# Kernel tuning notes

Measured on AMD Instinct MI355X. Metric: run time of the kernel, lower is better.

The kernel has to match this reference:

```python
import jax, jax.numpy as jnp
import numpy as np

D_MODEL = 1024
NUM_HEADS = 16
D_K = D_MODEL // NUM_HEADS


def setup_inputs() -> dict:
    key = jax.random.key(0)
    ks = jax.random.split(key, 11)
    B, S = 2, 2048
    scale = 1.0 / np.sqrt(D_MODEL)
    inp = {
        "q": jax.random.normal(ks[0], (B, S, D_MODEL), jnp.float32),
        "k": jax.random.normal(ks[1], (B, S, D_MODEL), jnp.float32),
        "v": jax.random.normal(ks[2], (B, S, D_MODEL), jnp.float32),
        "wq": jax.random.normal(ks[3], (D_MODEL, D_MODEL), jnp.float32) * scale,
        "bq": jax.random.normal(ks[4], (D_MODEL,), jnp.float32) * 0.01,
        "wk": jax.random.normal(ks[5], (D_MODEL, D_MODEL), jnp.float32) * scale,
        "bk": jax.random.normal(ks[6], (D_MODEL,), jnp.float32) * 0.01,
        "wv": jax.random.normal(ks[7], (D_MODEL, D_MODEL), jnp.float32) * scale,
        "bv": jax.random.normal(ks[8], (D_MODEL,), jnp.float32) * 0.01,
        "wo": jax.random.normal(ks[9], (D_MODEL, D_MODEL), jnp.float32) * scale,
        "bo": jax.random.normal(ks[10], (D_MODEL,), jnp.float32) * 0.01,
    }
    return inp


def reference(q, k, v, wq, bq, wk, bk, wv, bv, wo, bo):
    B, S, _ = q.shape
    # Linear projections (torch Linear: x @ W.T + b). Weights stored [out, in].
    qh = (q @ wq.T + bq).reshape(B, S, NUM_HEADS, D_K).transpose(0, 2, 1, 3)  # [B,H,S,dk]
    kh = (k @ wk.T + bk).reshape(B, S, NUM_HEADS, D_K).transpose(0, 2, 1, 3)
    vh = (v @ wv.T + bv).reshape(B, S, NUM_HEADS, D_K).transpose(0, 2, 1, 3)
    scores = jnp.einsum("bhqd,bhkd->bhqk", qh, kh) / jnp.sqrt(jnp.asarray(D_K, qh.dtype))
    weights = jax.nn.softmax(scores, axis=-1)
    attn = jnp.einsum("bhqk,bhkd->bhqd", weights, vh)  # [B,H,S,dk]
    attn = attn.transpose(0, 2, 1, 3).reshape(B, S, D_MODEL)
    return attn @ wo.T + bo
```

## Files before the change

kernel.cpp:

```cpp
#include <hip/hip_runtime.h>

#define DM 1024
#define NH 16
#define DK 64
#define BB 2
#define SS 2048
#define MT (BB*SS)

typedef __attribute__((ext_vector_type(8))) short bf16x8;
typedef __attribute__((ext_vector_type(4))) float f32x4;

#define QSCALE 0.1803368801111191f
#define EXPC  (-14.426950408889634f)

__device__ __forceinline__ unsigned short f2bf(float f) {
    unsigned int u = __float_as_uint(f);
    u += 0x7FFF + ((u >> 16) & 1);
    return (unsigned short)(u >> 16);
}

__device__ __forceinline__ unsigned int cvt_pk_bf16(float lo, float hi) {
    unsigned int r;
    asm("v_cvt_pk_bf16_f32 %0, %1, %2" : "=v"(r) : "v"(lo), "v"(hi));
    return r;
}

__device__ __forceinline__ void gload16(const void* g, void* l) {
    __builtin_amdgcn_global_load_lds(
        (const __attribute__((address_space(1))) unsigned int*)g,
        (__attribute__((address_space(3))) unsigned int*)(unsigned int)(unsigned long long)l,
        16, 0, 0);
}

__device__ __forceinline__ int kperm(int s) {
    return (s & ~31) | (((s >> 2) & 1) << 4) | (((s >> 3) & 3) << 2) | (s & 3);
}

struct CvtArgs {
    const float* s[7];
    unsigned short* d[7];
    int n[7];
    float scl[7];
};

__global__ __launch_bounds__(256) void cvt_f32_bf16(CvtArgs a) {
    const int arr = blockIdx.y;
    const int i = (blockIdx.x * 256 + threadIdx.x) * 8;
    if (i >= a.n[arr]) return;
    const float sc = a.scl[arr];
    const float4* sp = (const float4*)(a.s[arr] + i);
    float4 x = sp[0], y = sp[1];
    union { unsigned short us[8]; uint4 u4; } r;
    r.us[0] = f2bf(x.x * sc); r.us[1] = f2bf(x.y * sc);
    r.us[2] = f2bf(x.z * sc); r.us[3] = f2bf(x.w * sc);
    r.us[4] = f2bf(y.x * sc); r.us[5] = f2bf(y.y * sc);
    r.us[6] = f2bf(y.z * sc); r.us[7] = f2bf(y.w * sc);
    *(uint4*)(a.d[arr] + i) = r.u4;
}

struct ProjArgs {
    const unsigned short* A[3];
    const unsigned short* B[3];
    const float* bias[3];
    unsigned short* out[3];
    float bscale[3];
};

__global__ __launch_bounds__(256, 3) void proj3(ProjArgs pa) {
    __shared__ __align__(16) unsigned short As[2][128 * 32];
    __shared__ __align__(16) unsigned short Bs[2][128 * 32];

    const int z = blockIdx.y;
    const int bx = blockIdx.x;
    const int m0 = (z < 2 ? (bx >> 3) : (bx >> 5)) * 128;
    const int n0 = (z < 2 ? (bx & 7) : (bx & 31)) * 128;
    const unsigned short* A = pa.A[z];
    const unsigned short* B = pa.B[z];
    const float* bias = pa.bias[z];
    const float bsc = pa.bscale[z];
    unsigned short* out = pa.out[z];

    const int tid = (int)threadIdx.x;
    const int l = tid & 63;
    const int w = tid >> 6;
    const int wm = w >> 1, wn = w & 1;

    const int strow = l >> 2;
    const int sslot = (l & 3) ^ ((l >> 3) & 3);
    const int fr = l & 15, fj = l >> 4;
    const int swz = ((fj ^ ((fr >> 1) & 3)) << 4);

    const f32x4 zero = {0.f, 0.f, 0.f, 0.f};
    f32x4 acc[4][4];
    #pragma unroll
    for (int mf = 0; mf < 4; ++mf)
        #pragma unroll
        for (int nf = 0; nf < 4; ++nf) acc[mf][nf] = zero;

    #pragma unroll
    for (int t = 0; t < 2; ++t) {
        const int c = w * 2 + t;
        const int row = c * 16 + strow;
        gload16(A + (size_t)(m0 + row) * DM + sslot * 8, (char*)As[0] + c * 1024);
        gload16(B + (size_t)(n0 + row) * DM + sslot * 8, (char*)Bs[0] + c * 1024);
    }
    __syncthreads();

    for (int kt = 0; kt < DM; kt += 32) {
        const int cb = (kt >> 5) & 1;
        if (kt + 32 < DM) {
            #pragma unroll
            for (int t = 0; t < 2; ++t) {
                const int c = w * 2 + t;
                const int row = c * 16 + strow;
                gload16(A + (size_t)(m0 + row) * DM + (kt + 32) + sslot * 8, (char*)As[cb ^ 1] + c * 1024);
                gload16(B + (size_t)(n0 + row) * DM + (kt + 32) + sslot * 8, (char*)Bs[cb ^ 1] + c * 1024);
            }
        }
        bf16x8 af[4], bfr[4];
        #pragma unroll
        for (int mf = 0; mf < 4; ++mf)
            af[mf] = *(const bf16x8*)((const char*)As[cb] + (wm * 64 + mf * 16 + fr) * 64 + swz);
        #pragma unroll
        for (int nf = 0; nf < 4; ++nf)
            bfr[nf] = *(const bf16x8*)((const char*)Bs[cb] + (wn * 64 + nf * 16 + fr) * 64 + swz);
        #pragma unroll
        for (int mf = 0; mf < 4; ++mf)
            #pragma unroll
            for (int nf = 0; nf < 4; ++nf)
                acc[mf][nf] = __builtin_amdgcn_mfma_f32_16x16x32_bf16(af[mf], bfr[nf], acc[mf][nf], 0, 0, 0);
        __syncthreads();
    }

    #pragma unroll
    for (int nf = 0; nf < 4; ++nf) {
        const int n = n0 + wn * 64 + nf * 16 + fr;
        const float bn = (z == 2) ? 0.f : bias[n] * bsc;
        #pragma unroll
        for (int mf = 0; mf < 4; ++mf) {
            #pragma unroll
            for (int j = 0; j < 4; ++j) {
                const int m = m0 + wm * 64 + mf * 16 + fj * 4 + j;
                if (z < 2) {
                    const float val = acc[mf][nf][j] + bn;
                    int s = m & (SS - 1);
                    if (z == 1) s = kperm(s);
                    out[((size_t)((m >> 11) * NH + (n >> 6)) * SS + s) * DK + (n & 63)] = f2bf(val);
                } else {
                    const float val = acc[mf][nf][j] + bias[m];
                    out[(size_t)((n >> 11) * NH + (m >> 6)) * (SS * DK) + (size_t)(m & 63) * SS + (n & (SS - 1))] = f2bf(val);
                }
            }
        }
    }
}

__global__ __launch_bounds__(256, 2) void gemm_out(
    const unsigned short* __restrict__ A,
    const unsigned short* __restrict__ B,
    const float* __restrict__ bias,
    float* __restrict__ out)
{
    __shared__ __align__(16) unsigned short As[2][128 * 32];
    __shared__ __align__(16) unsigned short Bs[2][64 * 32];

    const int tid = (int)threadIdx.x;
    const int l = tid & 63;
    const int w = tid >> 6;
    const int wm = w >> 1, wn = w & 1;
    const int m0 = blockIdx.x * 128, n0 = blockIdx.y * 64;

    const int strow = l >> 2;
    const int sslot = (l & 3) ^ ((l >> 3) & 3);
    const int fr = l & 15, fj = l >> 4;
    const int swz = ((fj ^ ((fr >> 1) & 3)) << 4);

    const f32x4 zero = {0.f, 0.f, 0.f, 0.f};
    f32x4 acc[4][2];
    #pragma unroll
    for (int mf = 0; mf < 4; ++mf)
        #pragma unroll
        for (int nf = 0; nf < 2; ++nf) acc[mf][nf] = zero;

    #pragma unroll
    for (int t = 0; t < 2; ++t) {
        const int c = w * 2 + t;
        gload16(A + (size_t)(m0 + c * 16 + strow) * DM + sslot * 8, (char*)As[0] + c * 1024);
    }
    gload16(B + (size_t)(n0 + w * 16 + strow) * DM + sslot * 8, (char*)Bs[0] + w * 1024);
    __syncthreads();

    for (int kt = 0; kt < DM; kt += 32) {
        const int cb = (kt >> 5) & 1;
        if (kt + 32 < DM) {
            #pragma unroll
            for (int t = 0; t < 2; ++t) {
                const int c = w * 2 + t;
                gload16(A + (size_t)(m0 + c * 16 + strow) * DM + (kt + 32) + sslot * 8, (char*)As[cb ^ 1] + c * 1024);
            }
            gload16(B + (size_t)(n0 + w * 16 + strow) * DM + (kt + 32) + sslot * 8, (char*)Bs[cb ^ 1] + w * 1024);
        }
        bf16x8 af[4], bfr[2];
        #pragma unroll
        for (int mf = 0; mf < 4; ++mf)
            af[mf] = *(const bf16x8*)((const char*)As[cb] + (wm * 64 + mf * 16 + fr) * 64 + swz);
        #pragma unroll
        for (int nf = 0; nf < 2; ++nf)
            bfr[nf] = *(const bf16x8*)((const char*)Bs[cb] + (wn * 32 + nf * 16 + fr) * 64 + swz);
        #pragma unroll
        for (int mf = 0; mf < 4; ++mf)
            #pragma unroll
            for (int nf = 0; nf < 2; ++nf)
                acc[mf][nf] = __builtin_amdgcn_mfma_f32_16x16x32_bf16(af[mf], bfr[nf], acc[mf][nf], 0, 0, 0);
        __syncthreads();
    }

    #pragma unroll
    for (int nf = 0; nf < 2; ++nf) {
        const int n = n0 + wn * 32 + nf * 16 + fr;
        const float bn = bias[n];
        #pragma unroll
        for (int mf = 0; mf < 4; ++mf)
            #pragma unroll
            for (int j = 0; j < 4; ++j) {
                const int m = m0 + wm * 64 + mf * 16 + fj * 4 + j;
                out[(size_t)m * DM + n] = acc[mf][nf][j] + bn;
            }
    }
}

__global__ __launch_bounds__(256, 2) void attn_bf16(
    const unsigned short* __restrict__ qh,
    const unsigned short* __restrict__ kh,
    const unsigned short* __restrict__ vt,
    unsigned short* __restrict__ ao)
{
    __shared__ __align__(16) unsigned short Ks[2][64 * 64];
    __shared__ __align__(16) unsigned short Vs[2][64 * 64];

    const int tid = (int)threadIdx.x;
    const int l = tid & 63;
    const int w = tid >> 6;
    const int bh = blockIdx.x;
    const int q0 = blockIdx.y * 128;
    const size_t pb = (size_t)bh * (SS * DK);

    const int fr = l & 15, fj = l >> 4;
    const int s8 = fr & 7;
    const int strow = l >> 3;
    const int sslot = (l & 7) ^ strow;

    bf16x8 qreg[2][2];
    #pragma unroll
    for (int qf = 0; qf < 2; ++qf)
        #pragma unroll
        for (int ks = 0; ks < 2; ++ks)
            qreg[qf][ks] = *(const bf16x8*)(qh + pb + (size_t)(q0 + w * 32 + qf * 16 + fr) * DK + ks * 32 + fj * 8);

    #pragma unroll
    for (int t = 0; t < 2; ++t) {
        const int c = w * 2 + t;
        gload16(kh + pb + (size_t)(c * 8 + strow) * DK + sslot * 8, (char*)Ks[0] + c * 1024);
        gload16(vt + pb + (size_t)(c * 8 + strow) * SS + sslot * 8, (char*)Vs[0] + c * 1024);
    }
    asm volatile("s_waitcnt vmcnt(0)" ::: "memory");
    __syncthreads();

    const f32x4 zero = {0.f, 0.f, 0.f, 0.f};
    f32x4 ot[4][2];
    f32x4 lacc[2];
    #pragma unroll
    for (int nf = 0; nf < 4; ++nf)
        #pragma unroll
        for (int qf = 0; qf < 2; ++qf) ot[nf][qf] = zero;
    lacc[0] = zero; lacc[1] = zero;

    const int NT = SS / 64;
    for (int t = 0; t < NT; ++t) {
        const int c = t & 1;
        if (t + 1 < NT) {
            #pragma unroll
            for (int tt = 0; tt < 2; ++tt) {
                const int ch = w * 2 + tt;
                gload16(kh + pb + (size_t)((t + 1) * 64 + ch * 8 + strow) * DK + sslot * 8,
                        (char*)Ks[c ^ 1] + ch * 1024);
            }
        }
        f32x4 sc[4][2];
        #pragma unroll
        for (int kf = 0; kf < 4; ++kf)
            #pragma unroll
            for (int qf = 0; qf < 2; ++qf) sc[kf][qf] = zero;
        __builtin_amdgcn_s_setprio(1);
        #pragma unroll
        for (int ks = 0; ks < 2; ++ks) {
            bf16x8 kfr[4];
            #pragma unroll
            for (int kf = 0; kf < 4; ++kf)
                kfr[kf] = *(const bf16x8*)((const char*)Ks[c] + (kf * 16 + fr) * 128 + (((ks * 4 + fj) ^ s8) << 4));
            #pragma unroll
            for (int kf = 0; kf < 4; ++kf)
                #pragma unroll
                for (int qf = 0; qf < 2; ++qf)
                    sc[kf][qf] = __builtin_amdgcn_mfma_f32_16x16x32_bf16(kfr[kf], qreg[qf][ks], sc[kf][qf], 0, 0, 0);
        }
        __builtin_amdgcn_s_setprio(0);

        bf16x8 pbf[2][2];
        #pragma unroll
        for (int qf = 0; qf < 2; ++qf) {
            #pragma unroll
            for (int ks = 0; ks < 2; ++ks) {
                union { unsigned int u[4]; bf16x8 v; } pk;
                #pragma unroll
                for (int kf = 0; kf < 2; ++kf) {
                    const f32x4 s4 = sc[ks * 2 + kf][qf];
                    const float e0 = __builtin_amdgcn_exp2f(s4[0] + EXPC);
                    const float e1 = __builtin_amdgcn_exp2f(s4[1] + EXPC);
                    const float e2 = __builtin_amdgcn_exp2f(s4[2] + EXPC);
                    const float e3 = __builtin_amdgcn_exp2f(s4[3] + EXPC);
                    lacc[qf][0] += e0; lacc[qf][1] += e1;
                    lacc[qf][2] += e2; lacc[qf][3] += e3;
                    pk.u[kf * 2 + 0] = cvt_pk_bf16(e0, e1);
                    pk.u[kf * 2 + 1] = cvt_pk_bf16(e2, e3);
                }
                pbf[qf][ks] = pk.v;
            }
        }

        __builtin_amdgcn_sched_barrier(0);
        asm volatile("s_waitcnt vmcnt(0) lgkmcnt(0)" ::: "memory");
        __builtin_amdgcn_s_barrier();
        __builtin_amdgcn_sched_barrier(0);

        if (t + 1 < NT) {
            #pragma unroll
            for (int tt = 0; tt < 2; ++tt) {
                const int ch = w * 2 + tt;
                gload16(vt + pb + (size_t)(ch * 8 + strow) * SS + (t + 1) * 64 + sslot * 8,
                        (char*)Vs[c ^ 1] + ch * 1024);
            }
        }

        __builtin_amdgcn_s_setprio(1);
        #pragma unroll
        for (int ks = 0; ks < 2; ++ks) {
            bf16x8 va[4];
            #pragma unroll
            for (int nf = 0; nf < 4; ++nf)
                va[nf] = *(const bf16x8*)((const char*)Vs[c] + (nf * 16 + fr) * 128 + (((ks * 4 + fj) ^ s8) << 4));
            #pragma unroll
            for (int nf = 0; nf < 4; ++nf)
                #pragma unroll
                for (int qf = 0; qf < 2; ++qf)
                    ot[nf][qf] = __builtin_amdgcn_mfma_f32_16x16x32_bf16(va[nf], pbf[qf][ks], ot[nf][qf], 0, 0, 0);
        }
        __builtin_amdgcn_s_setprio(0);
    }

    float inv[2];
    #pragma unroll
    for (int qf = 0; qf < 2; ++qf) {
        float s = (lacc[qf][0] + lacc[qf][1]) + (lacc[qf][2] + lacc[qf][3]);
        s += __shfl_xor(s, 16);
        s += __shfl_xor(s, 32);
        inv[qf] = 1.0f / s;
    }
    const int b = bh >> 4, h = bh & 15;
    #pragma unroll
    for (int qf = 0; qf < 2; ++qf) {
        const int qg = q0 + w * 32 + qf * 16 + fr;
        unsigned short* dst = ao + (size_t)(b * SS + qg) * DM + h * DK + fj * 4;
        #pragma unroll
        for (int nf = 0; nf < 4; ++nf) {
            uint2 pw;
            pw.x = cvt_pk_bf16(ot[nf][qf][0] * inv[qf], ot[nf][qf][1] * inv[qf]);
            pw.y = cvt_pk_bf16(ot[nf][qf][2] * inv[qf], ot[nf][qf][3] * inv[qf]);
            *(uint2*)(dst + nf * 16) = pw;
        }
    }
}

extern "C" void kernel_launch(void* const* d_in, const int* in_sizes, int n_in,
                              void* d_out, int out_size, void* d_ws, size_t ws_size,
                              hipStream_t stream) {
    const float* q  = (const float*)d_in[0];
    const float* k  = (const float*)d_in[1];
    const float* v  = (const float*)d_in[2];
    const float* wq = (const float*)d_in[3];
    const float* bq = (const float*)d_in[4];
    const float* wk = (const float*)d_in[5];
    const float* bk = (const float*)d_in[6];
    const float* wv = (const float*)d_in[7];
    const float* bv = (const float*)d_in[8];
    const float* wo = (const float*)d_in[9];
    const float* bo = (const float*)d_in[10];

    const size_t NQ = (size_t)MT * DM;
    const size_t NW = (size_t)DM * DM;
    unsigned short* wsb = (unsigned short*)d_ws;
    unsigned short* qb  = wsb;
    unsigned short* kb  = qb  + NQ;
    unsigned short* vb  = kb  + NQ;
    unsigned short* wqb = vb  + NQ;
    unsigned short* wkb = wqb + NW;
    unsigned short* wvb = wkb + NW;
    unsigned short* wob = wvb + NW;
    unsigned short* qhb = wob + NW;
    unsigned short* khb = qhb + NQ;
    unsigned short* vtb = khb + NQ;
    unsigned short* aob = vtb + NQ;

    CvtArgs ca;
    ca.s[0] = q;  ca.d[0] = qb;  ca.n[0] = (int)NQ; ca.scl[0] = 1.f;
    ca.s[1] = k;  ca.d[1] = kb;  ca.n[1] = (int)NQ; ca.scl[1] = 1.f;
    ca.s[2] = v;  ca.d[2] = vb;  ca.n[2] = (int)NQ; ca.scl[2] = 1.f;
    ca.s[3] = wq; ca.d[3] = wqb; ca.n[3] = (int)NW; ca.scl[3] = QSCALE;
    ca.s[4] = wk; ca.d[4] = wkb; ca.n[4] = (int)NW; ca.scl[4] = 1.f;
    ca.s[5] = wv; ca.d[5] = wvb; ca.n[5] = (int)NW; ca.scl[5] = 1.f;
    ca.s[6] = wo; ca.d[6] = wob; ca.n[6] = (int)NW; ca.scl[6] = 1.f;
    cvt_f32_bf16<<<dim3(2048, 7), dim3(256), 0, stream>>>(ca);

    ProjArgs pa;
    pa.A[0] = qb;  pa.B[0] = wqb; pa.bias[0] = bq; pa.out[0] = qhb; pa.bscale[0] = QSCALE;
    pa.A[1] = kb;  pa.B[1] = wkb; pa.bias[1] = bk; pa.out[1] = khb; pa.bscale[1] = 1.f;
    pa.A[2] = wvb; pa.B[2] = vb;  pa.bias[2] = bv; pa.out[2] = vtb; pa.bscale[2] = 1.f;
    proj3<<<dim3(256, 3), dim3(256), 0, stream>>>(pa);

    attn_bf16<<<dim3(32, 16), dim3(256), 0, stream>>>(qhb, khb, vtb, aob);

    gemm_out<<<dim3(32, 16), dim3(256), 0, stream>>>(aob, wob, bo, (float*)d_out);
}
```

Measured before the change: 119.0 us.

## Fuse fp32-to-bf16 activation conversion into projection GEMM loads; remap blocks per XCD

The separate conversion pass over the q, k and v activations is removed. The projection GEMM now reads the fp32 activation tiles straight into registers, packs them to bf16 with v_cvt_pk_bf16 and writes them to LDS after the MFMA block, while the weight operand still uses direct global-to-LDS loads. This saves a full write and re-read of three bf16 activation copies plus most of the cvt kernel's work. Block indices are also remapped so that blocks sharing an XCD (bx&7) cover neighbouring M/N tiles, for better L2 reuse. The cost is higher register pressure and exposed global-load latency on the fp32 path, since those loads are no longer asynchronous into LDS.

```diff
diff --git a/kernel.cpp b/kernel.cpp
--- a/kernel.cpp
+++ b/kernel.cpp
@@ -37,16 +37,14 @@
 }
 
 struct CvtArgs {
-    const float* s[7];
-    unsigned short* d[7];
-    int n[7];
-    float scl[7];
+    const float* s[4];
+    unsigned short* d[4];
+    float scl[4];
 };
 
 __global__ __launch_bounds__(256) void cvt_f32_bf16(CvtArgs a) {
     const int arr = blockIdx.y;
     const int i = (blockIdx.x * 256 + threadIdx.x) * 8;
-    if (i >= a.n[arr]) return;
     const float sc = a.scl[arr];
     const float4* sp = (const float4*)(a.s[arr] + i);
     float4 x = sp[0], y = sp[1];
@@ -59,8 +57,8 @@
 }
 
 struct ProjArgs {
-    const unsigned short* A[3];
-    const unsigned short* B[3];
+    const void* A[3];
+    const void* B[3];
     const float* bias[3];
     unsigned short* out[3];
     float bscale[3];
@@ -72,10 +70,17 @@
 
     const int z = blockIdx.y;
     const int bx = blockIdx.x;
-    const int m0 = (z < 2 ? (bx >> 3) : (bx >> 5)) * 128;
-    const int n0 = (z < 2 ? (bx & 7) : (bx & 31)) * 128;
-    const unsigned short* A = pa.A[z];
-    const unsigned short* B = pa.B[z];
+    const int xcd = bx & 7, ib = bx >> 3;
+    int mb, nb;
+    if (z < 2) { mb = xcd * 4 + (ib >> 3); nb = ib & 7; }
+    else       { mb = ib >> 2;             nb = xcd * 4 + (ib & 3); }
+    const int m0 = mb * 128, n0 = nb * 128;
+
+    const bool a32 = (z < 2);
+    const float* Af = (const float*)pa.A[z];
+    const unsigned short* Ab = (const unsigned short*)pa.A[z];
+    const float* Bf = (const float*)pa.B[z];
+    const unsigned short* Bb = (const unsigned short*)pa.B[z];
     const float* bias = pa.bias[z];
     const float bsc = pa.bscale[z];
     unsigned short* out = pa.out[z];
@@ -101,20 +106,46 @@
     for (int t = 0; t < 2; ++t) {
         const int c = w * 2 + t;
         const int row = c * 16 + strow;
-        gload16(A + (size_t)(m0 + row) * DM + sslot * 8, (char*)As[0] + c * 1024);
-        gload16(B + (size_t)(n0 + row) * DM + sslot * 8, (char*)Bs[0] + c * 1024);
+        const int col = sslot * 8;
+        if (a32) {
+            const float4* s = (const float4*)(Af + (size_t)(m0 + row) * DM + col);
+            float4 f0 = s[0], f1 = s[1];
+            union { unsigned int u[4]; bf16x8 v; } pk;
+            pk.u[0] = cvt_pk_bf16(f0.x, f0.y); pk.u[1] = cvt_pk_bf16(f0.z, f0.w);
+            pk.u[2] = cvt_pk_bf16(f1.x, f1.y); pk.u[3] = cvt_pk_bf16(f1.z, f1.w);
+            *(bf16x8*)((char*)As[0] + c * 1024 + l * 16) = pk.v;
+            gload16(Bb + (size_t)(n0 + row) * DM + col, (char*)Bs[0] + c * 1024);
+        } else {
+            gload16(Ab + (size_t)(m0 + row) * DM + col, (char*)As[0] + c * 1024);
+            const float4* s = (const float4*)(Bf + (size_t)(n0 + row) * DM + col);
+            float4 f0 = s[0], f1 = s[1];
+            union { unsigned int u[4]; bf16x8 v; } pk;
+            pk.u[0] = cvt_pk_bf16(f0.x, f0.y); pk.u[1] = cvt_pk_bf16(f0.z, f0.w);
+            pk.u[2] = cvt_pk_bf16(f1.x, f1.y); pk.u[3] = cvt_pk_bf16(f1.z, f1.w);
+            *(bf16x8*)((char*)Bs[0] + c * 1024 + l * 16) = pk.v;
+        }
     }
     __syncthreads();
 
     for (int kt = 0; kt < DM; kt += 32) {
         const int cb = (kt >> 5) & 1;
-        if (kt + 32 < DM) {
+        const bool pf = (kt + 32 < DM);
+        float4 rf[2][2];
+        if (pf) {
             #pragma unroll
             for (int t = 0; t < 2; ++t) {
                 const int c = w * 2 + t;
                 const int row = c * 16 + strow;
-                gload16(A + (size_t)(m0 + row) * DM + (kt + 32) + sslot * 8, (char*)As[cb ^ 1] + c * 1024);
-                gload16(B + (size_t)(n0 + row) * DM + (kt + 32) + sslot * 8, (char*)Bs[cb ^ 1] + c * 1024);
+                const int col = kt + 32 + sslot * 8;
+                if (a32) {
+                    const float4* s = (const float4*)(Af + (size_t)(m0 + row) * DM + col);
+                    rf[t][0] = s[0]; rf[t][1] = s[1];
+                    gload16(Bb + (size_t)(n0 + row) * DM + col, (char*)Bs[cb ^ 1] + c * 1024);
+                } else {
+                    gload16(Ab + (size_t)(m0 + row) * DM + col, (char*)As[cb ^ 1] + c * 1024);
+                    const float4* s = (const float4*)(Bf + (size_t)(n0 + row) * DM + col);
+                    rf[t][0] = s[0]; rf[t][1] = s[1];
+                }
             }
         }
         bf16x8 af[4], bfr[4];
@@ -129,6 +160,19 @@
             #pragma unroll
             for (int nf = 0; nf < 4; ++nf)
                 acc[mf][nf] = __builtin_amdgcn_mfma_f32_16x16x32_bf16(af[mf], bfr[nf], acc[mf][nf], 0, 0, 0);
+        if (pf) {
+            #pragma unroll
+            for (int t = 0; t < 2; ++t) {
+                const int c = w * 2 + t;
+                union { unsigned int u[4]; bf16x8 v; } pk;
+                pk.u[0] = cvt_pk_bf16(rf[t][0].x, rf[t][0].y);
+                pk.u[1] = cvt_pk_bf16(rf[t][0].z, rf[t][0].w);
+                pk.u[2] = cvt_pk_bf16(rf[t][1].x, rf[t][1].y);
+                pk.u[3] = cvt_pk_bf16(rf[t][1].z, rf[t][1].w);
+                if (a32) *(bf16x8*)((char*)As[cb ^ 1] + c * 1024 + l * 16) = pk.v;
+                else     *(bf16x8*)((char*)Bs[cb ^ 1] + c * 1024 + l * 16) = pk.v;
+            }
+        }
         __syncthreads();
     }
 
@@ -399,10 +443,7 @@
     const size_t NQ = (size_t)MT * DM;
     const size_t NW = (size_t)DM * DM;
     unsigned short* wsb = (unsigned short*)d_ws;
-    unsigned short* qb  = wsb;
-    unsigned short* kb  = qb  + NQ;
-    unsigned short* vb  = kb  + NQ;
-    unsigned short* wqb = vb  + NQ;
+    unsigned short* wqb = wsb;
     unsigned short* wkb = wqb + NW;
     unsigned short* wvb = wkb + NW;
     unsigned short* wob = wvb + NW;
@@ -412,19 +453,16 @@
     unsigned short* aob = vtb + NQ;
 
     CvtArgs ca;
-    ca.s[0] = q;  ca.d[0] = qb;  ca.n[0] = (int)NQ; ca.scl[0] = 1.f;
-    ca.s[1] = k;  ca.d[1] = kb;  ca.n[1] = (int)NQ; ca.scl[1] = 1.f;
-    ca.s[2] = v;  ca.d[2] = vb;  ca.n[2] = (int)NQ; ca.scl[2] = 1.f;
-    ca.s[3] = wq; ca.d[3] = wqb; ca.n[3] = (int)NW; ca.scl[3] = QSCALE;
-    ca.s[4] = wk; ca.d[4] = wkb; ca.n[4] = (int)NW; ca.scl[4] = 1.f;
-    ca.s[5] = wv; ca.d[5] = wvb; ca.n[5] = (int)NW; ca.scl[5] = 1.f;
-    ca.s[6] = wo; ca.d[6] = wob; ca.n[6] = (int)NW; ca.scl[6] = 1.f;
-    cvt_f32_bf16<<<dim3(2048, 7), dim3(256), 0, stream>>>(ca);
+    ca.s[0] = wq; ca.d[0] = wqb; ca.scl[0] = QSCALE;
+    ca.s[1] = wk; ca.d[1] = wkb; ca.scl[1] = 1.f;
+    ca.s[2] = wv; ca.d[2] = wvb; ca.scl[2] = 1.f;
+    ca.s[3] = wo; ca.d[3] = wob; ca.scl[3] = 1.f;
+    cvt_f32_bf16<<<dim3(512, 4), dim3(256), 0, stream>>>(ca);
 
     ProjArgs pa;
-    pa.A[0] = qb;  pa.B[0] = wqb; pa.bias[0] = bq; pa.out[0] = qhb; pa.bscale[0] = QSCALE;
-    pa.A[1] = kb;  pa.B[1] = wkb; pa.bias[1] = bk; pa.out[1] = khb; pa.bscale[1] = 1.f;
-    pa.A[2] = wvb; pa.B[2] = vb;  pa.bias[2] = bv; pa.out[2] = vtb; pa.bscale[2] = 1.f;
+    pa.A[0] = q;   pa.B[0] = wqb; pa.bias[0] = bq; pa.out[0] = qhb; pa.bscale[0] = QSCALE;
+    pa.A[1] = k;   pa.B[1] = wkb; pa.bias[1] = bk; pa.out[1] = khb; pa.bscale[1] = 1.f;
+    pa.A[2] = wvb; pa.B[2] = v;   pa.bias[2] = bv; pa.out[2] = vtb; pa.bscale[2] = 1.f;
     proj3<<<dim3(256, 3), dim3(256), 0, stream>>>(pa);
 
     attn_bf16<<<dim3(32, 16), dim3(256), 0, stream>>>(qhb, khb, vtb, aob);
```

After: 112.4 us. -5.5%, faster.
